# Kernel optimization log

Measured on AMD Instinct MI355X. Metric: run time of the kernel, lower is better.

## Reference

```python
import jax, jax.numpy as jnp
import numpy as np
import math

B, T, C = 4, 2048, 768
N_HEAD = 12
HEAD_DIM = C // N_HEAD


def setup_inputs() -> dict:
    key = jax.random.key(0)
    k1, k2, k3, k4, k5 = jax.random.split(key, 5)
    std = 0.02
    x = jax.random.normal(k1, (B, T, C), dtype=jnp.float32)
    W_attn = jax.random.normal(k2, (C, 3 * C), dtype=jnp.float32) * std
    b_attn = jnp.zeros((3 * C,), dtype=jnp.float32)
    W_proj = jax.random.normal(k3, (C, C), dtype=jnp.float32) * std
    b_proj = jnp.zeros((C,), dtype=jnp.float32)
    return {"x": x, "W_attn": W_attn, "b_attn": b_attn,
            "W_proj": W_proj, "b_proj": b_proj}


def reference(x, W_attn, b_attn, W_proj, b_proj):
    b, t, c = x.shape
    h, hd = N_HEAD, c // N_HEAD
    # qkv projection: [B,T,3C] -> q,k,v each [B,H,T,hd]
    qkv = x @ W_attn + b_attn
    qkv = qkv.reshape(b, t, 3, h, hd).transpose(2, 0, 3, 1, 4)  # [3,B,H,T,hd]
    q, k, v = qkv[0], qkv[1], qkv[2]
    scale = 1.0 / math.sqrt(hd)
    # full T x T attention scores (non-flash, as in original)
    attn = jnp.einsum('bhqd,bhkd->bhqk', q, k) * scale  # [B,H,T,T]
    causal = jnp.tril(jnp.ones((t, t), dtype=bool))
    attn = jnp.where(causal[None, None, :, :], attn, -jnp.inf)
    attn = jax.nn.softmax(attn, axis=-1)
    y = jnp.einsum('bhqk,bhkd->bhqd', attn, v)  # [B,H,T,hd]
    y = y.transpose(0, 2, 1, 3).reshape(b, t, c)  # merge heads
    return y @ W_proj + b_proj
```

## Files before the change

### kernel.cpp

```cpp
#include <hip/hip_runtime.h>
#include <hip/hip_bf16.h>
#include <cstdint>

#define B_  4
#define T_  2048
#define C_  768
#define H_  12
#define HD_ 64

#define AS1 __attribute__((address_space(1)))
#define AS3 __attribute__((address_space(3)))

typedef float    f32x4  __attribute__((ext_vector_type(4)));
typedef __bf16   bf16x8 __attribute__((ext_vector_type(8)));
typedef uint32_t u32x4  __attribute__((ext_vector_type(4)));

#define QSCL 0.18033688011112042f

__device__ __forceinline__ uint16_t f2b(float f) {
  __bf16 h = (__bf16)f;
  return __builtin_bit_cast(uint16_t, h);
}
__device__ __forceinline__ uint32_t pk2(float a, float b) {
  return (uint32_t)f2b(a) | ((uint32_t)f2b(b) << 16);
}
__device__ __forceinline__ uint32_t cvtpk(float lo, float hi) {
  uint32_t r;
  asm("v_cvt_pk_bf16_f32 %0, %1, %2" : "=v"(r) : "v"(lo), "v"(hi));
  return r;
}

__global__ void k_cvt(const float* __restrict__ in, uint16_t* __restrict__ out, int n4) {
  int i = blockIdx.x * blockDim.x + threadIdx.x;
  if (i >= n4) return;
  float4 v = ((const float4*)in)[i];
  uint2 o;
  o.x = pk2(v.x, v.y);
  o.y = pk2(v.z, v.w);
  ((uint2*)out)[i] = o;
}

__global__ void k_tr2(const float* __restrict__ Wa, uint16_t* __restrict__ WtA,
                      const float* __restrict__ Wp, uint16_t* __restrict__ WtP) {
  __shared__ float tile[32][33];
  const int bx = blockIdx.x;
  const float* in;
  uint16_t* out;
  int Cc, n0;
  if (bx < 72) { in = Wa; out = WtA; Cc = 2304; n0 = bx * 32; }
  else         { in = Wp; out = WtP; Cc = 768;  n0 = (bx - 72) * 32; }
  const int k0 = blockIdx.y * 32;
  const int tx = threadIdx.x, ty = threadIdx.y;
#pragma unroll
  for (int i = 0; i < 32; i += 8)
    tile[ty + i][tx] = in[(size_t)(k0 + ty + i) * Cc + n0 + tx];
  __syncthreads();
#pragma unroll
  for (int i = 0; i < 32; i += 8)
    out[(size_t)(n0 + ty + i) * 768 + k0 + tx] = f2b(tile[tx][ty + i]);
}

template <int EPI>
__global__ __launch_bounds__(256, 3) void k_gemm(
    const uint16_t* __restrict__ A, const uint16_t* __restrict__ Bt,
    const float* __restrict__ bias, float* __restrict__ outF,
    uint16_t* __restrict__ outQKV, int M, int N, int K, int nY) {
  __shared__ __align__(16) uint16_t As[3][128 * 32];
  __shared__ __align__(16) uint16_t Bs[3][128 * 32];
  const int nwg = gridDim.x;
  const int bid = blockIdx.x;
  const int wgid = (bid & 7) * (nwg >> 3) + (bid >> 3);
  const int wy = wgid % nY, wx = wgid / nY;

  const int tid  = threadIdx.x;
  const int lane = tid & 63;
  const int wave = tid >> 6;
  const int wrow = (wave >> 1) * 64, wcol = (wave & 1) * 64;
  const int rowBase = wx * 128, colBase = wy * 128;
  const int l16 = lane & 15, kg = lane >> 4;

  f32x4 acc[4][4];
#pragma unroll
  for (int i = 0; i < 4; ++i)
#pragma unroll
    for (int j = 0; j < 4; ++j) acc[i][j] = (f32x4){0.f, 0.f, 0.f, 0.f};

  const int srow  = lane >> 2;
  const int sslot = lane & 3;
  const int ssw   = (sslot ^ (srow & 3)) << 3;

  auto STAGE = [&](int buf, int k0) {
#pragma unroll
    for (int i = 0; i < 2; ++i) {
      const int r = i * 64 + wave * 16 + srow;
      const uint16_t* srcA = A  + (size_t)(rowBase + r) * K + k0 + ssw;
      const uint16_t* srcB = Bt + (size_t)(colBase + r) * K + k0 + ssw;
      uint16_t* dstA = &As[buf][(i * 64 + wave * 16) * 32];
      uint16_t* dstB = &Bs[buf][(i * 64 + wave * 16) * 32];
      __builtin_amdgcn_global_load_lds((const AS1 uint32_t*)srcA, (AS3 uint32_t*)dstA, 16, 0, 0);
      __builtin_amdgcn_global_load_lds((const AS1 uint32_t*)srcB, (AS3 uint32_t*)dstB, 16, 0, 0);
    }
  };

  const int sA = (kg ^ (l16 & 3)) << 3;

  STAGE(0, 0);
  if (32 < K) STAGE(1, 32);
  int t = 0;
  for (int k0 = 0; k0 < K; k0 += 32, ++t) {
    if (k0 + 32 < K) {
      asm volatile("s_waitcnt vmcnt(4)" ::: "memory");
    } else {
      asm volatile("s_waitcnt vmcnt(0)" ::: "memory");
    }
    __builtin_amdgcn_sched_barrier(0);
    __builtin_amdgcn_s_barrier();

    if (k0 + 64 < K) STAGE((t + 2) % 3, k0 + 64);

    const int cb = t % 3;
    bf16x8 af[4], bfv[4];
#pragma unroll
    for (int mi = 0; mi < 4; ++mi)
      af[mi] = *(const bf16x8*)&As[cb][(wrow + mi * 16 + l16) * 32 + sA];
#pragma unroll
    for (int nj = 0; nj < 4; ++nj)
      bfv[nj] = *(const bf16x8*)&Bs[cb][(wcol + nj * 16 + l16) * 32 + sA];
#pragma unroll
    for (int mi = 0; mi < 4; ++mi)
#pragma unroll
      for (int nj = 0; nj < 4; ++nj)
        acc[mi][nj] = __builtin_amdgcn_mfma_f32_16x16x32_bf16(af[mi], bfv[nj], acc[mi][nj], 0, 0, 0);
  }

  const int rg = lane >> 4;
#pragma unroll
  for (int mi = 0; mi < 4; ++mi)
#pragma unroll
    for (int nj = 0; nj < 4; ++nj) {
      int c = colBase + wcol + nj * 16 + l16;
      float bv = bias[c];
      if (EPI == 0) {
#pragma unroll
        for (int jj = 0; jj < 4; ++jj) {
          int r = rowBase + wrow + mi * 16 + rg * 4 + jj;
          outF[(size_t)r * N + c] = acc[mi][nj][jj] + bv;
        }
      } else {
        int sel = c / 768;
        int rem = c - sel * 768;
        int head = rem >> 6, d = rem & 63;
        int r0 = rowBase + wrow + mi * 16 + rg * 4;
        int bb = r0 >> 11, tt0 = r0 & 2047;
        if (sel == 2) {
          size_t off = (((size_t)2 * (B_ * H_) + bb * H_ + head) * HD_ + d) * T_ + tt0;
          uint2 w;
          w.x = pk2(acc[mi][nj][0] + bv, acc[mi][nj][1] + bv);
          w.y = pk2(acc[mi][nj][2] + bv, acc[mi][nj][3] + bv);
          *(uint2*)&outQKV[off] = w;
        } else {
          float scl = (sel == 0) ? QSCL : 1.0f;
#pragma unroll
          for (int jj = 0; jj < 4; ++jj) {
            size_t off = (((size_t)sel * (B_ * H_) + bb * H_ + head) * T_ + tt0 + jj) * HD_ + d;
            outQKV[off] = f2b((acc[mi][nj][jj] + bv) * scl);
          }
        }
      }
    }
}

__global__ __launch_bounds__(512, 6) void k_attn2(
    const uint16_t* __restrict__ Qb, const uint16_t* __restrict__ Kb,
    const uint16_t* __restrict__ Vb, uint16_t* __restrict__ Y) {
  __shared__ __align__(16) uint16_t Ks[2][64 * 64];
  __shared__ __align__(16) uint16_t Vs[2][64 * 64];
  __shared__ __align__(16) uint32_t Pw[8][16 * 20];
  const int tid  = threadIdx.x;
  const int lane = tid & 63;
  const int wq   = tid >> 6;
  const int qw   = wq & 3;
  const int kh   = wq >> 2;
  const int l16  = lane & 15, kg = lane >> 4;

  const int idx = blockIdx.x;
  const int tq  = idx >> 3;
  const int px  = tq & 15;
  const int g   = (idx & 7) + 8 * (tq >> 4);
  const int h = g % H_, b = g / H_;
  const size_t headBase = ((size_t)(b * H_ + h)) * (size_t)(T_ * HD_);

  const int srow0 = tid >> 3;
  const int sslot = lane & 7;
  const int ssw   = ((sslot ^ (srow0 & 7)) << 3);

  uint32_t* pw = &Pw[wq][0];
  uint16_t* dstK0 = &Ks[0][(wq * 8) * 64];
  uint16_t* dstK1 = &Ks[1][(wq * 8) * 64];
  uint16_t* dstV0 = &Vs[0][(wq * 8) * 64];
  uint16_t* dstV1 = &Vs[1][(wq * 8) * 64];

  u32x4 onesw;
  onesw[0] = 0x3f803f80u; onesw[1] = 0x3f803f80u;
  onesw[2] = 0x3f803f80u; onesw[3] = 0x3f803f80u;
  const bf16x8 onesf = __builtin_bit_cast(bf16x8, onesw);

  int cur = 0;
  for (int part = 0; part < 2; ++part) {
    const int qb = part ? (31 - px) : px;
    const int qrow0 = qb * 64 + qw * 16;

    bf16x8 qf[2];
    {
      const uint16_t* qp = Qb + headBase + (size_t)(qrow0 + l16) * HD_;
      qf[0] = *(const bf16x8*)(qp + kg * 8);
      qf[1] = *(const bf16x8*)(qp + 32 + kg * 8);
    }

    f32x4 o[4];
#pragma unroll
    for (int i = 0; i < 4; ++i) o[i] = (f32x4){0.f, 0.f, 0.f, 0.f};
    f32x4 lq = (f32x4){0.f, 0.f, 0.f, 0.f};

    const uint16_t* kp = Kb + headBase + (size_t)srow0 * HD_ + ssw;
    const uint16_t* vp = Vb + headBase + (size_t)srow0 * T_ + ssw;

    auto STAGE = [&](int buf) {
      __builtin_amdgcn_global_load_lds((const AS1 uint32_t*)kp,
                                       (AS3 uint32_t*)(buf ? dstK1 : dstK0), 16, 0, 0);
      __builtin_amdgcn_global_load_lds((const AS1 uint32_t*)vp,
                                       (AS3 uint32_t*)(buf ? dstV1 : dstV0), 16, 0, 0);
      kp += 64 * HD_;
      vp += 64;
    };

    const int nt = qb + 1;
    __syncthreads();
    STAGE(cur);

    for (int t = 0; t < nt; ++t) {
      asm volatile("s_waitcnt vmcnt(0)" ::: "memory");
      __builtin_amdgcn_sched_barrier(0);
      __builtin_amdgcn_s_barrier();

      if (t + 1 < nt) STAGE(cur ^ 1);

      const uint16_t* KT = &Ks[cur][0];
      const uint16_t* VT = &Vs[cur][0];

      f32x4 sm[2];
      __builtin_amdgcn_s_setprio(1);
#pragma unroll
      for (int nj = 0; nj < 2; ++nj) {
        f32x4 acc = (f32x4){0.f, 0.f, 0.f, 0.f};
        const int row = kh * 32 + nj * 16 + l16;
#pragma unroll
        for (int kc = 0; kc < 2; ++kc) {
          const int s = (((kc * 4 + kg) ^ (row & 7)) << 3);
          bf16x8 kf = *(const bf16x8*)&KT[row * 64 + s];
          acc = __builtin_amdgcn_mfma_f32_16x16x32_bf16(kf, qf[kc], acc, 0, 0, 0);
        }
        sm[nj] = acc;
      }
      __builtin_amdgcn_s_setprio(0);

      if (t == qb) {
        const int kvb = t * 64 + kh * 32 + kg * 4;
        const int qg  = qrow0 + l16;
#pragma unroll
        for (int nj = 0; nj < 2; ++nj)
#pragma unroll
          for (int jj = 0; jj < 4; ++jj)
            if (kvb + nj * 16 + jj > qg) sm[nj][jj] = -__builtin_inff();
      }

#pragma unroll
      for (int nj = 0; nj < 2; ++nj)
#pragma unroll
        for (int jj = 0; jj < 4; ++jj)
          sm[nj][jj] = __builtin_exp2f(sm[nj][jj]);

#pragma unroll
      for (int nj = 0; nj < 2; ++nj) {
        uint2 w;
        w.x = cvtpk(sm[nj][0], sm[nj][1]);
        w.y = cvtpk(sm[nj][2], sm[nj][3]);
        *(uint2*)&pw[l16 * 20 + nj * 8 + kg * 2] = w;
      }

      __builtin_amdgcn_s_setprio(1);
      bf16x8 pa = *(const bf16x8*)&pw[l16 * 20 + kg * 4];
#pragma unroll
      for (int njd = 0; njd < 4; ++njd) {
        const int row = njd * 16 + l16;
        const int s = (((kh * 4 + kg) ^ (row & 7)) << 3);
        bf16x8 vf = *(const bf16x8*)&VT[row * 64 + s];
        o[njd] = __builtin_amdgcn_mfma_f32_16x16x32_bf16(vf, pa, o[njd], 0, 0, 0);
      }
      lq = __builtin_amdgcn_mfma_f32_16x16x32_bf16(onesf, pa, lq, 0, 0, 0);
      __builtin_amdgcn_s_setprio(0);

      cur ^= 1;
    }

    float l_ = lq[0];

    __syncthreads();
    f32x4* cO = (f32x4*)&Ks[0][0];
    float*  cL = (float*)&Vs[0][0];
    if (kh) {
#pragma unroll
      for (int njd = 0; njd < 4; ++njd) cO[(njd * 4 + qw) * 64 + lane] = o[njd];
      if (lane < 16) cL[qw * 64 + lane] = l_;
    }
    __syncthreads();
    if (!kh) {
      float lsum = l_ + cL[qw * 64 + l16];
      float inv = __builtin_amdgcn_rcpf(lsum);
      const int q = qrow0 + l16;
      uint16_t* yp = Y + ((size_t)(b * T_ + q)) * C_ + h * HD_ + kg * 4;
#pragma unroll
      for (int njd = 0; njd < 4; ++njd) {
        f32x4 oc = o[njd] + cO[(njd * 4 + qw) * 64 + lane];
        uint2 w;
        w.x = cvtpk(oc[0] * inv, oc[1] * inv);
        w.y = cvtpk(oc[2] * inv, oc[3] * inv);
        *(uint2*)(yp + njd * 16) = w;
      }
    }
  }
}

extern "C" void kernel_launch(void* const* d_in, const int* in_sizes, int n_in,
                              void* d_out, int out_size, void* d_ws, size_t ws_size,
                              hipStream_t stream) {
  const float* x      = (const float*)d_in[0];
  const float* W_attn = (const float*)d_in[1];
  const float* b_attn = (const float*)d_in[2];
  const float* W_proj = (const float*)d_in[3];
  const float* b_proj = (const float*)d_in[4];
  float* out = (float*)d_out;

  char* ws = (char*)d_ws;
  uint16_t* xb  = (uint16_t*)(ws);
  uint16_t* WtA = (uint16_t*)(ws + 12582912);
  uint16_t* WtP = (uint16_t*)(ws + 16121856);
  uint16_t* QKV = (uint16_t*)(ws + 17301504);
  uint16_t* Yb  = (uint16_t*)(ws + 55050240);

  uint16_t* Qp = QKV;
  uint16_t* Kp = QKV + 6291456;
  uint16_t* Vp = QKV + 12582912;

  k_cvt<<<6144, 256, 0, stream>>>(x, xb, 1572864);
  k_tr2<<<dim3(96, 24), dim3(32, 8), 0, stream>>>(W_attn, WtA, W_proj, WtP);
  k_gemm<1><<<1152, 256, 0, stream>>>(xb, WtA, b_attn, nullptr, QKV, 8192, 2304, 768, 18);
  k_attn2<<<768, 512, 0, stream>>>(Qp, Kp, Vp, Yb);
  k_gemm<0><<<384, 256, 0, stream>>>(Yb, WtP, b_proj, out, nullptr, 8192, 768, 768, 6);
}
```

Before: 130.7 us.

## Use 256x256-tile double-buffered GEMM kernel for the QKV projection

Replaces the 128x128-tile QKV GEMM (1152 blocks, 256 threads, triple buffer) with a dedicated 256x256-tile kernel using 512 threads, K-tile 64, XOR-swizzled LDS, direct global-to-LDS loads and double buffering. Larger tiles raise arithmetic intensity and cut global reloads of A and B. Uses 128KB of LDS at one block per CU, so 288 blocks on 256 CUs leave a partial second wave and give less latency hiding.

```diff
diff --git a/kernel.cpp b/kernel.cpp
--- a/kernel.cpp
+++ b/kernel.cpp
@@ -58,6 +58,120 @@
 #pragma unroll
   for (int i = 0; i < 32; i += 8)
     out[(size_t)(n0 + ty + i) * 768 + k0 + tx] = f2b(tile[tx][ty + i]);
+}
+
+__global__ __launch_bounds__(512, 1) void k_gemm256(
+    const uint16_t* __restrict__ A, const uint16_t* __restrict__ Bt,
+    const float* __restrict__ bias, uint16_t* __restrict__ outQKV) {
+  __shared__ __align__(16) uint16_t As[2][256 * 64];
+  __shared__ __align__(16) uint16_t Bs[2][256 * 64];
+  const int tid  = threadIdx.x;
+  const int lane = tid & 63;
+  const int wq   = tid >> 6;
+  const int wm   = wq >> 2;
+  const int wn   = wq & 3;
+  const int l16  = lane & 15, kg = lane >> 4;
+
+  const int bid  = blockIdx.x;
+  const int wgid = (bid & 7) * 36 + (bid >> 3);
+  const int wx = wgid / 9, wy = wgid % 9;
+  const int rowBase = wx * 256, colBase = wy * 256;
+
+  f32x4 acc[8][4];
+#pragma unroll
+  for (int i = 0; i < 8; ++i)
+#pragma unroll
+    for (int j = 0; j < 4; ++j) acc[i][j] = (f32x4){0.f, 0.f, 0.f, 0.f};
+
+  const int srow  = tid >> 3;
+  const int sslot = tid & 7;
+  const int ssw   = ((sslot ^ (srow & 7)) << 3);
+
+  auto STAGE = [&](int buf, int kt) {
+    const int k0 = kt * 64;
+#pragma unroll
+    for (int j = 0; j < 4; ++j) {
+      const uint16_t* srcA = A + (size_t)(rowBase + j * 64 + srow) * 768 + k0 + ssw;
+      __builtin_amdgcn_global_load_lds((const AS1 uint32_t*)srcA,
+          (AS3 uint32_t*)&As[buf][(j * 64 + wq * 8) * 64], 16, 0, 0);
+    }
+#pragma unroll
+    for (int j = 0; j < 4; ++j) {
+      const uint16_t* srcB = Bt + (size_t)(colBase + j * 64 + srow) * 768 + k0 + ssw;
+      __builtin_amdgcn_global_load_lds((const AS1 uint32_t*)srcB,
+          (AS3 uint32_t*)&Bs[buf][(j * 64 + wq * 8) * 64], 16, 0, 0);
+    }
+  };
+
+  STAGE(0, 0);
+  for (int kt = 0; kt < 12; ++kt) {
+    const int g = kt & 1;
+    asm volatile("s_waitcnt vmcnt(0)" ::: "memory");
+    __builtin_amdgcn_sched_barrier(0);
+    __builtin_amdgcn_s_barrier();
+
+    if (kt + 1 < 12) STAGE(g ^ 1, kt + 1);
+
+    const uint16_t* AT = &As[g][0];
+    const uint16_t* BT = &Bs[g][0];
+#pragma unroll
+    for (int qm = 0; qm < 2; ++qm)
+#pragma unroll
+      for (int qn = 0; qn < 2; ++qn) {
+        bf16x8 af[4][2], bfv[2][2];
+#pragma unroll
+        for (int mi = 0; mi < 4; ++mi) {
+          const int row = wm * 128 + qm * 64 + mi * 16 + l16;
+#pragma unroll
+          for (int kc = 0; kc < 2; ++kc)
+            af[mi][kc] = *(const bf16x8*)&AT[row * 64 + (((kc * 4 + kg) ^ (row & 7)) << 3)];
+        }
+#pragma unroll
+        for (int nj = 0; nj < 2; ++nj) {
+          const int row = wn * 64 + qn * 32 + nj * 16 + l16;
+#pragma unroll
+          for (int kc = 0; kc < 2; ++kc)
+            bfv[nj][kc] = *(const bf16x8*)&BT[row * 64 + (((kc * 4 + kg) ^ (row & 7)) << 3)];
+        }
+        __builtin_amdgcn_s_setprio(1);
+#pragma unroll
+        for (int mi = 0; mi < 4; ++mi)
+#pragma unroll
+          for (int nj = 0; nj < 2; ++nj)
+#pragma unroll
+            for (int kc = 0; kc < 2; ++kc)
+              acc[qm * 4 + mi][qn * 2 + nj] = __builtin_amdgcn_mfma_f32_16x16x32_bf16(
+                  af[mi][kc], bfv[nj][kc], acc[qm * 4 + mi][qn * 2 + nj], 0, 0, 0);
+        __builtin_amdgcn_s_setprio(0);
+      }
+  }
+
+#pragma unroll
+  for (int mi = 0; mi < 8; ++mi)
+#pragma unroll
+    for (int nj = 0; nj < 4; ++nj) {
+      int c = colBase + wn * 64 + nj * 16 + l16;
+      float bv = bias[c];
+      int sel = c / 768;
+      int rem = c - sel * 768;
+      int head = rem >> 6, d = rem & 63;
+      int r0 = rowBase + wm * 128 + mi * 16 + kg * 4;
+      int bb = r0 >> 11, tt0 = r0 & 2047;
+      if (sel == 2) {
+        size_t off = (((size_t)2 * (B_ * H_) + bb * H_ + head) * HD_ + d) * T_ + tt0;
+        uint2 w;
+        w.x = pk2(acc[mi][nj][0] + bv, acc[mi][nj][1] + bv);
+        w.y = pk2(acc[mi][nj][2] + bv, acc[mi][nj][3] + bv);
+        *(uint2*)&outQKV[off] = w;
+      } else {
+        float scl = (sel == 0) ? QSCL : 1.0f;
+#pragma unroll
+        for (int jj = 0; jj < 4; ++jj) {
+          size_t off = (((size_t)sel * (B_ * H_) + bb * H_ + head) * T_ + tt0 + jj) * HD_ + d;
+          outQKV[off] = f2b((acc[mi][nj][jj] + bv) * scl);
+        }
+      }
+    }
 }
 
 template <int EPI>
@@ -354,7 +468,7 @@
 
   k_cvt<<<6144, 256, 0, stream>>>(x, xb, 1572864);
   k_tr2<<<dim3(96, 24), dim3(32, 8), 0, stream>>>(W_attn, WtA, W_proj, WtP);
-  k_gemm<1><<<1152, 256, 0, stream>>>(xb, WtA, b_attn, nullptr, QKV, 8192, 2304, 768, 18);
+  k_gemm256<<<288, 512, 0, stream>>>(xb, WtA, b_attn, QKV);
   k_attn2<<<768, 512, 0, stream>>>(Qp, Kp, Vp, Yb);
   k_gemm<0><<<384, 256, 0, stream>>>(Yb, WtP, b_proj, out, nullptr, 8192, 768, 768, 6);
 }
```

After: 140.1 us. 7.2% more time.
